# Kernel optimization log

Hardware: AMD Instinct MI355X
Metric: run time of the kernel (lower is better)

## Reference

```python
import jax, jax.numpy as jnp
import numpy as np

N_NODES, N_EDGES, IN_DIM, HID, N_FEAT_CLOSE, N_GRAPHS = 100000, 1600000, 128, 64, 5, 512


def _glorot(k, shape):
    lim = float(np.sqrt(6.0 / (shape[0] + shape[1])))
    return jax.random.uniform(k, shape, jnp.float32, -lim, lim)


def setup_inputs() -> dict:
    key = jax.random.key(0)
    ks = jax.random.split(key, 16)
    x = jax.random.normal(ks[0], (N_NODES, IN_DIM), jnp.float32)
    edge_index = jax.random.randint(ks[1], (2, N_EDGES), 0, N_NODES, jnp.int32)
    closeness = jax.random.uniform(ks[2], (N_NODES, N_FEAT_CLOSE), jnp.float32)
    batch = jnp.sort(jax.random.randint(ks[3], (N_NODES,), 0, N_GRAPHS, jnp.int32))
    return {
        'x': x, 'edge_index': edge_index, 'closeness': closeness, 'batch': batch,
        'num_graphs': N_GRAPHS,
        'W1': _glorot(ks[4], (IN_DIM, HID)), 'b1': jnp.zeros((HID,), jnp.float32),
        'W2': _glorot(ks[5], (HID, HID)), 'b2': jnp.zeros((HID,), jnp.float32),
        'W3': _glorot(ks[6], (HID, HID)), 'b3': jnp.zeros((HID,), jnp.float32),
        'Wc': _glorot(ks[7], (N_FEAT_CLOSE, 1)), 'bc': jnp.zeros((1,), jnp.float32),
        'Wa1': _glorot(ks[8], (HID, 16)), 'ba1': jnp.zeros((16,), jnp.float32),
        'Wa2': _glorot(ks[9], (16, 1)), 'ba2': jnp.zeros((1,), jnp.float32),
    }


def reference(x, edge_index, closeness, batch, num_graphs, W1, b1, W2, b2, W3, b3, Wc, bc, Wa1, ba1, Wa2, ba2):
    src, dst = edge_index[0], edge_index[1]
    N = x.shape[0]
    # GCN symmetric normalization with implicit self-loops (weight 1)
    deg = jax.ops.segment_sum(jnp.ones(src.shape, x.dtype), dst, num_segments=N) + 1.0
    dinv = jax.lax.rsqrt(deg)
    norm = dinv[src] * dinv[dst]  # [E]
    self_norm = (dinv * dinv)[:, None]  # 1/deg, self-loop coefficient

    def gcn(h, W, b):
        h = h @ W  # [N, hid]
        agg = jax.ops.segment_sum(h[src] * norm[:, None], dst, num_segments=N)
        return jax.nn.relu(agg + h * self_norm + b)

    h = gcn(x, W1, b1)
    h = gcn(h, W2, b2)
    h = gcn(h, W3, b3)

    # per-graph softmax over closeness scores, scaled by graph size
    s = closeness @ Wc + bc  # [N,1]
    smax = jax.ops.segment_max(s, batch, num_segments=num_graphs)
    e = jnp.exp(s - smax[batch])
    ssum = jax.ops.segment_sum(e, batch, num_segments=num_graphs)
    counts = jax.ops.segment_sum(jnp.ones((N,), x.dtype), batch, num_segments=num_graphs)
    w = (e / ssum[batch]) * counts[batch][:, None]  # [N,1]

    # weighted per-graph max pooling, then tiny MLP per graph
    pooled = jax.ops.segment_max(w * h, batch, num_segments=num_graphs)  # [G,64]
    a = jax.nn.relu(pooled @ Wa1 + ba1)
    return a @ Wa2 + ba2  # [G,1]
```

## Files before the change

### kernel.cpp

```cpp
#include <hip/hip_runtime.h>

#define N_NODESC 100000
#define N_EDGESC 1600000
#define IN_DIMC 128
#define HIDC 64
#define N_GRAPHSC 512
#define PAD_DEG 64


__global__ void zero_bounds_kernel(int* __restrict__ cntR, const int* __restrict__ batch,
                                   int* __restrict__ gstart) {
  int i = blockIdx.x * blockDim.x + threadIdx.x;
  if (i >= N_NODESC) return;
  cntR[i] = 0;
  cntR[N_NODESC + i] = 0;
  cntR[2 * N_NODESC + i] = 0;
  cntR[3 * N_NODESC + i] = 0;
  int b = batch[i];
  int prev = (i == 0) ? -1 : batch[i - 1];
  for (int g = prev + 1; g <= b; ++g) gstart[g] = i;
  if (i == N_NODESC - 1)
    for (int g = b + 1; g <= N_GRAPHSC; ++g) gstart[g] = N_NODESC;
}

__global__ void deg_kernel(const int* __restrict__ dstv, int* __restrict__ cntR,
                           int* __restrict__ slot) {
  int e4 = (blockIdx.x * blockDim.x + threadIdx.x) * 4;
  if (e4 >= N_EDGESC) return;
  int4 d = *(const int4*)(dstv + e4);
  int4 s;
  s.x = atomicAdd(&cntR[d.x], 1);
  s.y = atomicAdd(&cntR[N_NODESC + d.y], 1);
  s.z = atomicAdd(&cntR[2 * N_NODESC + d.z], 1);
  s.w = atomicAdd(&cntR[3 * N_NODESC + d.w], 1);
  *(int4*)(slot + e4) = s;
}

__global__ void off_dinv_kernel(const int* __restrict__ cntR, int* __restrict__ offR,
                                int* __restrict__ cnt, float* __restrict__ dinv) {
  int i = blockIdx.x * blockDim.x + threadIdx.x;
  if (i >= N_NODESC) return;
  int c0 = cntR[i];
  int c1 = cntR[N_NODESC + i];
  int c2 = cntR[2 * N_NODESC + i];
  int c3 = cntR[3 * N_NODESC + i];
  offR[i] = c0;
  offR[N_NODESC + i] = c0 + c1;
  offR[2 * N_NODESC + i] = c0 + c1 + c2;
  int tot = c0 + c1 + c2 + c3;
  cnt[i] = tot;
  dinv[i] = rsqrtf((float)tot + 1.0f);
}

__global__ void fill_pad_kernel(const int* __restrict__ srcv, const int* __restrict__ dstv,
                                const int* __restrict__ slot, const int* __restrict__ offR,
                                int* __restrict__ csr_pad) {
  int e4 = (blockIdx.x * blockDim.x + threadIdx.x) * 4;
  if (e4 >= N_EDGESC) return;
  int4 s = *(const int4*)(srcv + e4);
  int4 d = *(const int4*)(dstv + e4);
  int4 sl = *(const int4*)(slot + e4);
  int p0 = sl.x;
  int p1 = offR[d.y] + sl.y;
  int p2 = offR[N_NODESC + d.z] + sl.z;
  int p3 = offR[2 * N_NODESC + d.w] + sl.w;
  if (p0 < PAD_DEG) __builtin_nontemporal_store(s.x, &csr_pad[d.x * PAD_DEG + p0]);
  if (p1 < PAD_DEG) __builtin_nontemporal_store(s.y, &csr_pad[d.y * PAD_DEG + p1]);
  if (p2 < PAD_DEG) __builtin_nontemporal_store(s.z, &csr_pad[d.z * PAD_DEG + p2]);
  if (p3 < PAD_DEG) __builtin_nontemporal_store(s.w, &csr_pad[d.w * PAD_DEG + p3]);
}


#define GT_M 128
#define XS_LD 132
#define GT_BLOCKS ((N_NODESC + GT_M - 1) / GT_M)

template <int KT>
__global__ void __launch_bounds__(256, 3)
gemm_tile_kernel(const float* __restrict__ X, const float* __restrict__ W,
                 const float* __restrict__ dinv, float* __restrict__ T) {
  __shared__ float xs[64 * XS_LD];
  __shared__ float ws[64 * 64];
  int t = threadIdx.x;
  int base = blockIdx.x * GT_M;
  int r0 = (t >> 4) * 8;
  int c0 = (t & 15) * 4;
  float acc[8][4];
#pragma unroll
  for (int i = 0; i < 8; ++i)
#pragma unroll
    for (int j = 0; j < 4; ++j) acc[i][j] = 0.f;

  int kq = (t & 15) * 4;
  int rr = t >> 4;

  for (int kb = 0; kb < KT; kb += 64) {
    if (kb) __syncthreads();
#pragma unroll
    for (int it = 0; it < 8; ++it) {
      int r = rr + it * 16;
      int grow = base + r;
      if (grow >= N_NODESC) grow = N_NODESC - 1;
      float4 q = *(const float4*)(X + (size_t)grow * KT + kb + kq);
      xs[(kq + 0) * XS_LD + r] = q.x;
      xs[(kq + 1) * XS_LD + r] = q.y;
      xs[(kq + 2) * XS_LD + r] = q.z;
      xs[(kq + 3) * XS_LD + r] = q.w;
    }
#pragma unroll
    for (int it = 0; it < 4; ++it) {
      int idx = (it * 256 + t) * 4;
      *(float4*)(ws + idx) = *(const float4*)(W + (size_t)kb * HIDC + idx);
    }
    __syncthreads();
#pragma unroll 8
    for (int k = 0; k < 64; ++k) {
      float4 xa = *(const float4*)(xs + k * XS_LD + r0);
      float4 xb = *(const float4*)(xs + k * XS_LD + r0 + 4);
      float4 wf = *(const float4*)(ws + k * 64 + c0);
      float xf[8] = {xa.x, xa.y, xa.z, xa.w, xb.x, xb.y, xb.z, xb.w};
      float wv[4] = {wf.x, wf.y, wf.z, wf.w};
#pragma unroll
      for (int i = 0; i < 8; ++i)
#pragma unroll
        for (int j = 0; j < 4; ++j) acc[i][j] = fmaf(xf[i], wv[j], acc[i][j]);
    }
  }
#pragma unroll
  for (int i = 0; i < 8; ++i) {
    int row = base + r0 + i;
    if (row < N_NODESC) {
      float dv = dinv[row];
      float4 o;
      o.x = acc[i][0] * dv;
      o.y = acc[i][1] * dv;
      o.z = acc[i][2] * dv;
      o.w = acc[i][3] * dv;
      *(float4*)(T + (size_t)row * HIDC + c0) = o;
    }
  }
}

__global__ void gather_kernel(const float* __restrict__ ts, const float* __restrict__ dinv,
                              const int* __restrict__ cnt, const int* __restrict__ csr_pad,
                              const float* __restrict__ bias, float* __restrict__ h) {
  int lane = threadIdx.x & 63;
  int node = (blockIdx.x * blockDim.x + threadIdx.x) >> 6;
  if (node >= N_NODESC) return;
  int q = lane >> 4;
  int c = lane & 15;
  int deg = min(cnt[node], PAD_DEG);
  const int* __restrict__ row = csr_pad + node * PAD_DEG;
  const float4* __restrict__ ts4 = (const float4*)ts;
  float4 acc = make_float4(0.f, 0.f, 0.f, 0.f);
  int e = 0;
  for (; e + 16 <= deg; e += 16) {
    int s0 = row[e + q];
    int s1 = row[e + 4 + q];
    int s2 = row[e + 8 + q];
    int s3 = row[e + 12 + q];
    float4 v0 = ts4[s0 * 16 + c];
    float4 v1 = ts4[s1 * 16 + c];
    float4 v2 = ts4[s2 * 16 + c];
    float4 v3 = ts4[s3 * 16 + c];
    acc.x += (v0.x + v1.x) + (v2.x + v3.x);
    acc.y += (v0.y + v1.y) + (v2.y + v3.y);
    acc.z += (v0.z + v1.z) + (v2.z + v3.z);
    acc.w += (v0.w + v1.w) + (v2.w + v3.w);
  }
  for (; e + 4 <= deg; e += 4) {
    int s0 = row[e + q];
    float4 v = ts4[s0 * 16 + c];
    acc.x += v.x;
    acc.y += v.y;
    acc.z += v.z;
    acc.w += v.w;
  }
  if (e < deg && q < deg - e) {
    int s0 = row[e + q];
    float4 v = ts4[s0 * 16 + c];
    acc.x += v.x;
    acc.y += v.y;
    acc.z += v.z;
    acc.w += v.w;
  }
  acc.x += __shfl_xor(acc.x, 16);
  acc.y += __shfl_xor(acc.y, 16);
  acc.z += __shfl_xor(acc.z, 16);
  acc.w += __shfl_xor(acc.w, 16);
  acc.x += __shfl_xor(acc.x, 32);
  acc.y += __shfl_xor(acc.y, 32);
  acc.z += __shfl_xor(acc.z, 32);
  acc.w += __shfl_xor(acc.w, 32);
  if (q == 0) {
    float4 self = ts4[node * 16 + c];
    float4 bv = ((const float4*)bias)[c];
    float dv = dinv[node];
    float4 o;
    o.x = fmaxf(fmaf(acc.x + self.x, dv, bv.x), 0.f);
    o.y = fmaxf(fmaf(acc.y + self.y, dv, bv.y), 0.f);
    o.z = fmaxf(fmaf(acc.z + self.z, dv, bv.z), 0.f);
    o.w = fmaxf(fmaf(acc.w + self.w, dv, bv.w), 0.f);
    ((float4*)h)[node * 16 + c] = o;
  }
}

__global__ void __launch_bounds__(256)
readout_kernel(const float* __restrict__ h, const float* __restrict__ closeness,
               const float* __restrict__ Wc, const float* __restrict__ bc,
               const int* __restrict__ gstart, const float* __restrict__ Wa1,
               const float* __restrict__ ba1, const float* __restrict__ Wa2,
               const float* __restrict__ ba2, float* __restrict__ out) {
  __shared__ float sArr[1024];
  __shared__ float red[256];
  __shared__ float cross[4 * 64];
  int g = blockIdx.x;
  int t = threadIdx.x;
  int n0 = gstart[g], n1 = gstart[g + 1];
  int count = n1 - n0;
  int cap = min(count, 1024);
  float wc0 = Wc[0], wc1 = Wc[1], wc2 = Wc[2], wc3 = Wc[3], wc4 = Wc[4], bcv = bc[0];
  float lmax = -3.4e38f;
  for (int idx = t; idx < cap; idx += 256) {
    const float* c = closeness + (size_t)(n0 + idx) * 5;
    float s = fmaf(c[4], wc4, fmaf(c[3], wc3, fmaf(c[2], wc2, fmaf(c[1], wc1, fmaf(c[0], wc0, bcv)))));
    sArr[idx] = s;
    lmax = fmaxf(lmax, s);
  }
  red[t] = lmax;
  __syncthreads();
  for (int s = 128; s > 0; s >>= 1) {
    if (t < s) red[t] = fmaxf(red[t], red[t + s]);
    __syncthreads();
  }
  float m = red[0];
  __syncthreads();
  float lsum = 0.f;
  for (int idx = t; idx < cap; idx += 256) {
    float e = expf(sArr[idx] - m);
    sArr[idx] = e;
    lsum += e;
  }
  red[t] = lsum;
  __syncthreads();
  for (int s = 128; s > 0; s >>= 1) {
    if (t < s) red[t] += red[t + s];
    __syncthreads();
  }
  float scale = (count > 0) ? ((float)count / red[0]) : 0.f;
  __syncthreads();
  int wv = t >> 6, lane = t & 63;
  float pmax = 0.f;
  for (int idx = wv; idx < cap; idx += 4) {
    float w = sArr[idx] * scale;
    pmax = fmaxf(pmax, w * h[(size_t)(n0 + idx) * HIDC + lane]);
  }
  cross[wv * 64 + lane] = pmax;
  __syncthreads();
  if (wv == 0) {
    float p = fmaxf(fmaxf(cross[lane], cross[64 + lane]),
                    fmaxf(cross[128 + lane], cross[192 + lane]));
    float o = 0.f;
#pragma unroll
    for (int tt = 0; tt < 16; ++tt) {
      float prod = p * Wa1[lane * 16 + tt];
#pragma unroll
      for (int off = 32; off > 0; off >>= 1) prod += __shfl_xor(prod, off);
      float a = fmaxf(prod + ba1[tt], 0.f);
      o += a * Wa2[tt];
    }
    if (lane == 0) out[g] = o + ba2[0];
  }
}


extern "C" void kernel_launch(void* const* d_in, const int* in_sizes, int n_in,
                              void* d_out, int out_size, void* d_ws, size_t ws_size,
                              hipStream_t stream) {
  const float* x = (const float*)d_in[0];
  const int* ei = (const int*)d_in[1];
  const float* closeness = (const float*)d_in[2];
  const int* batch = (const int*)d_in[3];
  const float* W1 = (const float*)d_in[5];
  const float* b1 = (const float*)d_in[6];
  const float* W2 = (const float*)d_in[7];
  const float* b2 = (const float*)d_in[8];
  const float* W3 = (const float*)d_in[9];
  const float* b3 = (const float*)d_in[10];
  const float* Wc = (const float*)d_in[11];
  const float* bc = (const float*)d_in[12];
  const float* Wa1 = (const float*)d_in[13];
  const float* ba1 = (const float*)d_in[14];
  const float* Wa2 = (const float*)d_in[15];
  const float* ba2 = (const float*)d_in[16];
  float* out = (float*)d_out;
  const int* srcv = ei;
  const int* dstv = ei + N_EDGESC;

  char* ws = (char*)d_ws;
  size_t off = 0;
  auto alloc = [&](size_t bytes) -> void* {
    void* p = ws + off;
    off = (off + bytes + 255) & ~(size_t)255;
    return p;
  };
  float* tbuf = (float*)alloc(sizeof(float) * N_NODESC * HIDC);
  float* hbuf = (float*)alloc(sizeof(float) * N_NODESC * HIDC);
  int* csr_pad = (int*)alloc(sizeof(int) * N_NODESC * PAD_DEG);
  int* slot = (int*)alloc(sizeof(int) * N_EDGESC);
  int* cntR = (int*)alloc(sizeof(int) * N_NODESC * 4);
  int* offR = (int*)alloc(sizeof(int) * N_NODESC * 3);
  int* cnt = (int*)alloc(sizeof(int) * N_NODESC);
  float* dinv = (float*)alloc(sizeof(float) * N_NODESC);
  int* gstart = (int*)alloc(sizeof(int) * (N_GRAPHSC + 1));

  const int B = 256;
  int gN = (N_NODESC + B - 1) / B;
  int gE4 = (N_EDGESC / 4 + B - 1) / B;
  int gGather = (N_NODESC * 64) / B;

  zero_bounds_kernel<<<gN, B, 0, stream>>>(cntR, batch, gstart);
  deg_kernel<<<gE4, B, 0, stream>>>(dstv, cntR, slot);
  off_dinv_kernel<<<gN, B, 0, stream>>>(cntR, offR, cnt, dinv);
  fill_pad_kernel<<<gE4, B, 0, stream>>>(srcv, dstv, slot, offR, csr_pad);

  gemm_tile_kernel<IN_DIMC><<<GT_BLOCKS, B, 0, stream>>>(x, W1, dinv, tbuf);
  gather_kernel<<<gGather, B, 0, stream>>>(tbuf, dinv, cnt, csr_pad, b1, hbuf);
  gemm_tile_kernel<HIDC><<<GT_BLOCKS, B, 0, stream>>>(hbuf, W2, dinv, tbuf);
  gather_kernel<<<gGather, B, 0, stream>>>(tbuf, dinv, cnt, csr_pad, b2, hbuf);
  gemm_tile_kernel<HIDC><<<GT_BLOCKS, B, 0, stream>>>(hbuf, W3, dinv, tbuf);
  gather_kernel<<<gGather, B, 0, stream>>>(tbuf, dinv, cnt, csr_pad, b3, hbuf);

  readout_kernel<<<N_GRAPHSC, B, 0, stream>>>(hbuf, closeness, Wc, bc, gstart,
                                              Wa1, ba1, Wa2, ba2, out);
}
```

Before: 517.0 us.

## Fuse closeness softmax into degree kernel and replace tiled GEMM with per-row GEMM

The per-graph closeness softmax now runs as extra blocks inside the degree-counting kernel and writes per-node weights, so the readout kernel only does the weighted max-pool and the MLP. The shared-memory tiled GEMM is replaced by a one-row-per-thread kernel that holds the input row in registers and keeps the whole weight matrix in LDS. The first GEMM is moved ahead of the CSR fill. The goal is to cut serial work in the readout and simplify the GEMM, at the cost of heavy register use (a KT=128 row in registers) and uncoalesced per-thread row loads.

Result: slower. 637.8 us (+23.4%).

```diff
diff --git a/kernel.cpp b/kernel.cpp
--- a/kernel.cpp
+++ b/kernel.cpp
@@ -23,17 +23,62 @@
     for (int g = b + 1; g <= N_GRAPHSC; ++g) gstart[g] = N_NODESC;
 }
 
-__global__ void deg_kernel(const int* __restrict__ dstv, int* __restrict__ cntR,
-                           int* __restrict__ slot) {
-  int e4 = (blockIdx.x * blockDim.x + threadIdx.x) * 4;
-  if (e4 >= N_EDGESC) return;
-  int4 d = *(const int4*)(dstv + e4);
-  int4 s;
-  s.x = atomicAdd(&cntR[d.x], 1);
-  s.y = atomicAdd(&cntR[N_NODESC + d.y], 1);
-  s.z = atomicAdd(&cntR[2 * N_NODESC + d.z], 1);
-  s.w = atomicAdd(&cntR[3 * N_NODESC + d.w], 1);
-  *(int4*)(slot + e4) = s;
+#define DW_DEG_B 1563
+__global__ void __launch_bounds__(256)
+degw_kernel(const int* __restrict__ dstv, int* __restrict__ cntR, int* __restrict__ slot,
+            const float* __restrict__ closeness, const float* __restrict__ Wc,
+            const float* __restrict__ bc, const int* __restrict__ gstart,
+            float* __restrict__ wexp) {
+  __shared__ float sArr[1024];
+  __shared__ float red[256];
+  int bid = blockIdx.x;
+  int t = threadIdx.x;
+  if (bid < DW_DEG_B) {
+    int e4 = (bid * 256 + t) * 4;
+    if (e4 >= N_EDGESC) return;
+    int4 d = *(const int4*)(dstv + e4);
+    int4 s;
+    s.x = atomicAdd(&cntR[d.x], 1);
+    s.y = atomicAdd(&cntR[N_NODESC + d.y], 1);
+    s.z = atomicAdd(&cntR[2 * N_NODESC + d.z], 1);
+    s.w = atomicAdd(&cntR[3 * N_NODESC + d.w], 1);
+    *(int4*)(slot + e4) = s;
+    return;
+  }
+  int g = bid - DW_DEG_B;
+  int n0 = gstart[g], n1 = gstart[g + 1];
+  int count = n1 - n0;
+  int cap = min(count, 1024);
+  float wc0 = Wc[0], wc1 = Wc[1], wc2 = Wc[2], wc3 = Wc[3], wc4 = Wc[4], bcv = bc[0];
+  float lmax = -3.4e38f;
+  for (int idx = t; idx < cap; idx += 256) {
+    const float* c = closeness + (size_t)(n0 + idx) * 5;
+    float s = fmaf(c[4], wc4, fmaf(c[3], wc3, fmaf(c[2], wc2, fmaf(c[1], wc1, fmaf(c[0], wc0, bcv)))));
+    sArr[idx] = s;
+    lmax = fmaxf(lmax, s);
+  }
+  red[t] = lmax;
+  __syncthreads();
+  for (int s = 128; s > 0; s >>= 1) {
+    if (t < s) red[t] = fmaxf(red[t], red[t + s]);
+    __syncthreads();
+  }
+  float m = red[0];
+  __syncthreads();
+  float lsum = 0.f;
+  for (int idx = t; idx < cap; idx += 256) {
+    float e = expf(sArr[idx] - m);
+    sArr[idx] = e;
+    lsum += e;
+  }
+  red[t] = lsum;
+  __syncthreads();
+  for (int s = 128; s > 0; s >>= 1) {
+    if (t < s) red[t] += red[t + s];
+    __syncthreads();
+  }
+  float scale = (count > 0) ? ((float)count / red[0]) : 0.f;
+  for (int idx = t; idx < cap; idx += 256) wexp[n0 + idx] = sArr[idx] * scale;
 }
 
 __global__ void off_dinv_kernel(const int* __restrict__ cntR, int* __restrict__ offR,
@@ -70,73 +115,71 @@
   if (p3 < PAD_DEG) __builtin_nontemporal_store(s.w, &csr_pad[d.w * PAD_DEG + p3]);
 }
 
-
-#define GT_M 128
-#define XS_LD 132
-#define GT_BLOCKS ((N_NODESC + GT_M - 1) / GT_M)
+#define GR_BLOCKS ((N_NODESC + 127) / 128)
 
 template <int KT>
-__global__ void __launch_bounds__(256, 3)
-gemm_tile_kernel(const float* __restrict__ X, const float* __restrict__ W,
-                 const float* __restrict__ dinv, float* __restrict__ T) {
-  __shared__ float xs[64 * XS_LD];
-  __shared__ float ws[64 * 64];
+__global__ void __launch_bounds__(128)
+gemm_row_kernel(const float* __restrict__ X, const float* __restrict__ W,
+                const float* __restrict__ dinv, float* __restrict__ T) {
+  __shared__ float ws[KT * HIDC];
   int t = threadIdx.x;
-  int base = blockIdx.x * GT_M;
-  int r0 = (t >> 4) * 8;
-  int c0 = (t & 15) * 4;
-  float acc[8][4];
-#pragma unroll
-  for (int i = 0; i < 8; ++i)
-#pragma unroll
-    for (int j = 0; j < 4; ++j) acc[i][j] = 0.f;
-
-  int kq = (t & 15) * 4;
-  int rr = t >> 4;
-
-  for (int kb = 0; kb < KT; kb += 64) {
-    if (kb) __syncthreads();
-#pragma unroll
-    for (int it = 0; it < 8; ++it) {
-      int r = rr + it * 16;
-      int grow = base + r;
-      if (grow >= N_NODESC) grow = N_NODESC - 1;
-      float4 q = *(const float4*)(X + (size_t)grow * KT + kb + kq);
-      xs[(kq + 0) * XS_LD + r] = q.x;
-      xs[(kq + 1) * XS_LD + r] = q.y;
-      xs[(kq + 2) * XS_LD + r] = q.z;
-      xs[(kq + 3) * XS_LD + r] = q.w;
+  int row = blockIdx.x * 128 + t;
+  int r = (row < N_NODESC) ? row : (N_NODESC - 1);
+
+  float4 xr[KT / 4];
+#pragma unroll
+  for (int i = 0; i < KT / 4; ++i)
+    xr[i] = *(const float4*)(X + (size_t)r * KT + i * 4);
+
+#pragma unroll
+  for (int f = t; f < KT * HIDC / 4; f += 128)
+    *(float4*)(ws + (size_t)f * 4) = *(const float4*)(W + (size_t)f * 4);
+  __syncthreads();
+
+  float dv = dinv[r];
+  bool valid = row < N_NODESC;
+  float* orow = T + (size_t)r * HIDC;
+
+#pragma unroll 1
+  for (int cb = 0; cb < 4; ++cb) {
+    const float* wp = ws + cb * 16;
+    float4 a0 = make_float4(0.f, 0.f, 0.f, 0.f);
+    float4 a1 = a0, a2 = a0, a3 = a0;
+#pragma unroll
+    for (int k = 0; k < KT; ++k) {
+      const float4 q = xr[k >> 2];
+      const float xv = ((k & 3) == 0) ? q.x : ((k & 3) == 1) ? q.y : ((k & 3) == 2) ? q.z : q.w;
+      float4 w0 = *(const float4*)(wp + k * HIDC);
+      float4 w1 = *(const float4*)(wp + k * HIDC + 4);
+      float4 w2 = *(const float4*)(wp + k * HIDC + 8);
+      float4 w3 = *(const float4*)(wp + k * HIDC + 12);
+      a0.x = fmaf(xv, w0.x, a0.x);
+      a0.y = fmaf(xv, w0.y, a0.y);
+      a0.z = fmaf(xv, w0.z, a0.z);
+      a0.w = fmaf(xv, w0.w, a0.w);
+      a1.x = fmaf(xv, w1.x, a1.x);
+      a1.y = fmaf(xv, w1.y, a1.y);
+      a1.z = fmaf(xv, w1.z, a1.z);
+      a1.w = fmaf(xv, w1.w, a1.w);
+      a2.x = fmaf(xv, w2.x, a2.x);
+      a2.y = fmaf(xv, w2.y, a2.y);
+      a2.z = fmaf(xv, w2.z, a2.z);
+      a2.w = fmaf(xv, w2.w, a2.w);
+      a3.x = fmaf(xv, w3.x, a3.x);
+      a3.y = fmaf(xv, w3.y, a3.y);
+      a3.z = fmaf(xv, w3.z, a3.z);
+      a3.w = fmaf(xv, w3.w, a3.w);
     }
-#pragma unroll
-    for (int it = 0; it < 4; ++it) {
-      int idx = (it * 256 + t) * 4;
-      *(float4*)(ws + idx) = *(const float4*)(W + (size_t)kb * HIDC + idx);
-    }
-    __syncthreads();
-#pragma unroll 8
-    for (int k = 0; k < 64; ++k) {
-      float4 xa = *(const float4*)(xs + k * XS_LD + r0);
-      float4 xb = *(const float4*)(xs + k * XS_LD + r0 + 4);
-      float4 wf = *(const float4*)(ws + k * 64 + c0);
-      float xf[8] = {xa.x, xa.y, xa.z, xa.w, xb.x, xb.y, xb.z, xb.w};
-      float wv[4] = {wf.x, wf.y, wf.z, wf.w};
-#pragma unroll
-      for (int i = 0; i < 8; ++i)
-#pragma unroll
-        for (int j = 0; j < 4; ++j) acc[i][j] = fmaf(xf[i], wv[j], acc[i][j]);
-    }
-  }
-#pragma unroll
-  for (int i = 0; i < 8; ++i) {
-    int row = base + r0 + i;
-    if (row < N_NODESC) {
-      float dv = dinv[row];
-      float4 o;
-      o.x = acc[i][0] * dv;
-      o.y = acc[i][1] * dv;
-      o.z = acc[i][2] * dv;
-      o.w = acc[i][3] * dv;
-      *(float4*)(T + (size_t)row * HIDC + c0) = o;
+    if (valid) {
+      float4 o0, o1, o2, o3;
+      o0.x = a0.x * dv; o0.y = a0.y * dv; o0.z = a0.z * dv; o0.w = a0.w * dv;
+      o1.x = a1.x * dv; o1.y = a1.y * dv; o1.z = a1.z * dv; o1.w = a1.w * dv;
+      o2.x = a2.x * dv; o2.y = a2.y * dv; o2.z = a2.z * dv; o2.w = a2.w * dv;
+      o3.x = a3.x * dv; o3.y = a3.y * dv; o3.z = a3.z * dv; o3.w = a3.w * dv;
+      *(float4*)(orow + cb * 16 + 0) = o0;
+      *(float4*)(orow + cb * 16 + 4) = o1;
+      *(float4*)(orow + cb * 16 + 8) = o2;
+      *(float4*)(orow + cb * 16 + 12) = o3;
     }
   }
 }
@@ -206,54 +249,19 @@
 }
 
 __global__ void __launch_bounds__(256)
-readout_kernel(const float* __restrict__ h, const float* __restrict__ closeness,
-               const float* __restrict__ Wc, const float* __restrict__ bc,
-               const int* __restrict__ gstart, const float* __restrict__ Wa1,
-               const float* __restrict__ ba1, const float* __restrict__ Wa2,
-               const float* __restrict__ ba2, float* __restrict__ out) {
-  __shared__ float sArr[1024];
-  __shared__ float red[256];
+readout2_kernel(const float* __restrict__ h, const float* __restrict__ wexp,
+                const int* __restrict__ gstart, const float* __restrict__ Wa1,
+                const float* __restrict__ ba1, const float* __restrict__ Wa2,
+                const float* __restrict__ ba2, float* __restrict__ out) {
   __shared__ float cross[4 * 64];
   int g = blockIdx.x;
   int t = threadIdx.x;
   int n0 = gstart[g], n1 = gstart[g + 1];
-  int count = n1 - n0;
-  int cap = min(count, 1024);
-  float wc0 = Wc[0], wc1 = Wc[1], wc2 = Wc[2], wc3 = Wc[3], wc4 = Wc[4], bcv = bc[0];
-  float lmax = -3.4e38f;
-  for (int idx = t; idx < cap; idx += 256) {
-    const float* c = closeness + (size_t)(n0 + idx) * 5;
-    float s = fmaf(c[4], wc4, fmaf(c[3], wc3, fmaf(c[2], wc2, fmaf(c[1], wc1, fmaf(c[0], wc0, bcv)))));
-    sArr[idx] = s;
-    lmax = fmaxf(lmax, s);
-  }
-  red[t] = lmax;
-  __syncthreads();
-  for (int s = 128; s > 0; s >>= 1) {
-    if (t < s) red[t] = fmaxf(red[t], red[t + s]);
-    __syncthreads();
-  }
-  float m = red[0];
-  __syncthreads();
-  float lsum = 0.f;
-  for (int idx = t; idx < cap; idx += 256) {
-    float e = expf(sArr[idx] - m);
-    sArr[idx] = e;
-    lsum += e;
-  }
-  red[t] = lsum;
-  __syncthreads();
-  for (int s = 128; s > 0; s >>= 1) {
-    if (t < s) red[t] += red[t + s];
-    __syncthreads();
-  }
-  float scale = (count > 0) ? ((float)count / red[0]) : 0.f;
-  __syncthreads();
+  int cap = min(n1 - n0, 1024);
   int wv = t >> 6, lane = t & 63;
   float pmax = 0.f;
   for (int idx = wv; idx < cap; idx += 4) {
-    float w = sArr[idx] * scale;
-    pmax = fmaxf(pmax, w * h[(size_t)(n0 + idx) * HIDC + lane]);
+    pmax = fmaxf(pmax, wexp[n0 + idx] * h[(size_t)(n0 + idx) * HIDC + lane]);
   }
   cross[wv * 64 + lane] = pmax;
   __syncthreads();
@@ -312,6 +320,7 @@
   int* offR = (int*)alloc(sizeof(int) * N_NODESC * 3);
   int* cnt = (int*)alloc(sizeof(int) * N_NODESC);
   float* dinv = (float*)alloc(sizeof(float) * N_NODESC);
+  float* wexp = (float*)alloc(sizeof(float) * N_NODESC);
   int* gstart = (int*)alloc(sizeof(int) * (N_GRAPHSC + 1));
 
   const int B = 256;
@@ -320,17 +329,17 @@
   int gGather = (N_NODESC * 64) / B;
 
   zero_bounds_kernel<<<gN, B, 0, stream>>>(cntR, batch, gstart);
-  deg_kernel<<<gE4, B, 0, stream>>>(dstv, cntR, slot);
+  degw_kernel<<<DW_DEG_B + N_GRAPHSC, B, 0, stream>>>(dstv, cntR, slot,
+                                                      closeness, Wc, bc, gstart, wexp);
   off_dinv_kernel<<<gN, B, 0, stream>>>(cntR, offR, cnt, dinv);
+  gemm_row_kernel<IN_DIMC><<<GR_BLOCKS, 128, 0, stream>>>(x, W1, dinv, tbuf);
   fill_pad_kernel<<<gE4, B, 0, stream>>>(srcv, dstv, slot, offR, csr_pad);
 
-  gemm_tile_kernel<IN_DIMC><<<GT_BLOCKS, B, 0, stream>>>(x, W1, dinv, tbuf);
   gather_kernel<<<gGather, B, 0, stream>>>(tbuf, dinv, cnt, csr_pad, b1, hbuf);
-  gemm_tile_kernel<HIDC><<<GT_BLOCKS, B, 0, stream>>>(hbuf, W2, dinv, tbuf);
+  gemm_row_kernel<HIDC><<<GR_BLOCKS, 128, 0, stream>>>(hbuf, W2, dinv, tbuf);
   gather_kernel<<<gGather, B, 0, stream>>>(tbuf, dinv, cnt, csr_pad, b2, hbuf);
-  gemm_tile_kernel<HIDC><<<GT_BLOCKS, B, 0, stream>>>(hbuf, W3, dinv, tbuf);
+  gemm_row_kernel<HIDC><<<GR_BLOCKS, 128, 0, stream>>>(hbuf, W3, dinv, tbuf);
   gather_kernel<<<gGather, B, 0, stream>>>(tbuf, dinv, cnt, csr_pad, b3, hbuf);
 
-  readout_kernel<<<N_GRAPHSC, B, 0, stream>>>(hbuf, closeness, Wc, bc, gstart,
-                                              Wa1, ba1, Wa2, ba2, out);
-}
+  readout2_kernel<<<N_GRAPHSC, B, 0, stream>>>(hbuf, wexp, gstart, Wa1, ba1, Wa2, ba2, out);
+}
```
